# Optimization experiments

Hardware: AMD Instinct MI355X
Metric: run time of the kernel (lower is better)

Reference implementation:

```python
import jax, jax.numpy as jnp
import numpy as np

EPS = 1e-8

def _cosine_rows(a, b):
    na = jnp.maximum(jnp.linalg.norm(a, axis=1), EPS)
    nb = jnp.maximum(jnp.linalg.norm(b, axis=1), EPS)
    return jnp.sum(a * b, axis=1) / (na * nb)


def setup_inputs() -> dict:
    key = jax.random.key(0)
    k1, k2 = jax.random.split(key)
    X = jax.random.normal(k1, (16384, 1024), dtype=jnp.float32)
    dictionary = jax.random.normal(k2, (4096, 1024), dtype=jnp.float32)
    descriptors = jnp.arange(4096, dtype=jnp.int64)
    return {"X": X, "dictionary": dictionary, "descriptors": descriptors, "k": 16}


def reference(X, dictionary, descriptors, k):
    # SOMP with centering=True, criterion='l1', pc=None (default forward path)
    orig_X = X
    std_orig_sum = jnp.sum(jnp.var(orig_X, axis=0, ddof=1))
    X_mean = jnp.mean(X, axis=0, keepdims=True)   # [1, D]
    Xc = X - X_mean                               # centered data [N, D]

    M = dictionary.shape[0]
    notchosen = jnp.ones((M,), dtype=X.dtype)
    residual = Xc
    chosen, evr, l2, cosine = [], [], [], []
    W = None
    recon = jnp.zeros_like(Xc)

    for i in range(k):  # k is a static Python int -> unrolled, per-step shapes static
        cross = residual @ dictionary.T           # [N, M] -- dominant memory traffic
        scores = jnp.sum(jnp.abs(cross * notchosen), axis=0)  # l1 criterion
        idx = jnp.argmax(scores)
        chosen.append(idx)
        notchosen = notchosen.at[idx].set(0)

        atoms = dictionary[jnp.stack(chosen)]     # [i+1, D], dynamic gather, static shape
        # least squares: min ||atoms.T @ W - Xc.T||  (full column rank -> normal eqs)
        G = atoms @ atoms.T                       # [i+1, i+1]
        W = jnp.linalg.solve(G, atoms @ Xc.T)     # [i+1, N]
        recon = (atoms.T @ W).T                   # [N, D]
        residual = Xc - recon

        rec_full = X_mean + recon
        evr.append(jnp.sum(jnp.var(rec_full, axis=0, ddof=1)) / std_orig_sum)
        cosine.append(jnp.mean(_cosine_rows(orig_X, rec_full)))
        l2.append(jnp.mean((orig_X - rec_full) ** 2))

    weights = jnp.linalg.norm(W, axis=1)          # [k]
    chosen_arr = jnp.stack(chosen)
    recon_out = X_mean + recon
    residual_out = Xc - recon                     # == X - recon_out
    return (recon_out, residual_out, chosen_arr, weights, W.T,
            jnp.stack(evr), jnp.stack(l2), jnp.stack(cosine))
```

## Files before the change

### kernel.cpp

```cpp
#include <hip/hip_runtime.h>
#include <math.h>

#define NROWS 16384
#define DIMK  1024
#define MDIC  4096
#define KSEL  16

#define OFF_RECON   0
#define OFF_RESID   ((size_t)NROWS*DIMK)
#define OFF_CHOSEN  ((size_t)2*NROWS*DIMK)
#define OFF_WEIGHTS (OFF_CHOSEN + 16)
#define OFF_WT      (OFF_WEIGHTS + 16)
#define OFF_EVR     (OFF_WT + (size_t)NROWS*KSEL)
#define OFF_L2      (OFF_EVR + 16)
#define OFF_COS     (OFF_L2 + 16)

typedef unsigned short u16;
typedef unsigned long long u64;
typedef __attribute__((ext_vector_type(8))) short short8;
typedef __attribute__((ext_vector_type(4))) float f32x4;

__device__ inline float blockReduce256f(float v) {
    __shared__ float ws_[4];
    #pragma unroll
    for (int off = 32; off > 0; off >>= 1) v += __shfl_down(v, off);
    __syncthreads();
    if ((threadIdx.x & 63) == 0) ws_[threadIdx.x >> 6] = v;
    __syncthreads();
    return ws_[0] + ws_[1] + ws_[2] + ws_[3];
}

__device__ inline void wredStore(double v, int k, int lane, int wv, double (*accS)[4]) {
    #pragma unroll
    for (int off = 32; off > 0; off >>= 1) v += __shfl_down(v, off);
    if (lane == 0) accS[k][wv] = v;
}

__device__ inline u16 f2bf(float f) {
    unsigned u = __float_as_uint(f);
    unsigned r = u + 0x7FFFu + ((u >> 16) & 1u);
    return (u16)(r >> 16);
}
__device__ inline float bf2f(u16 h) { return __uint_as_float(((unsigned)h) << 16); }

__global__ void k_init(float* notchosen, u64* amx, u64* statsAcc, u64* ctr2) {
    int m = blockIdx.x * 256 + threadIdx.x;
    if (m < MDIC) notchosen[m] = 1.0f;
    if (blockIdx.x == 0) {
        if (threadIdx.x < 40) statsAcc[threadIdx.x] = 0ULL;
        if (threadIdx.x < 2)  amx[threadIdx.x] = 0ULL;
        if (threadIdx.x == 0) *ctr2 = 0ULL;
    }
}

__global__ __launch_bounds__(256) void k_colstats(const float* __restrict__ X,
                                                  float* __restrict__ colpart,
                                                  float* __restrict__ sqpart) {
    int d  = blockIdx.x * 256 + threadIdx.x;
    int r0 = blockIdx.y * 256;
    float s = 0.f, sq = 0.f;
    for (int r = 0; r < 256; ++r) {
        float v = X[(size_t)(r0 + r) * DIMK + d];
        s += v; sq += v * v;
    }
    colpart[(size_t)blockIdx.y * DIMK + d] = s;
    __shared__ float red[256];
    red[threadIdx.x] = sq; __syncthreads();
    for (int off = 128; off > 0; off >>= 1) {
        if (threadIdx.x < off) red[threadIdx.x] += red[threadIdx.x + off];
        __syncthreads();
    }
    if (threadIdx.x == 0) sqpart[blockIdx.y * 4 + blockIdx.x] = red[0];
}

__global__ __launch_bounds__(1024) void k_reduce_mean(const float* __restrict__ colpart,
                                                      const float* __restrict__ sqpart,
                                                      float* __restrict__ xmean,
                                                      double* __restrict__ scal) {
    int d = threadIdx.x;
    double s = 0.0;
    for (int y = 0; y < 64; ++y) s += (double)colpart[(size_t)y * DIMK + d];
    float m = (float)(s / (double)NROWS);
    xmean[d] = m;
    __shared__ double red[1024];
    red[d] = (double)m * (double)m; __syncthreads();
    for (int off = 512; off > 0; off >>= 1) {
        if (d < off) red[d] += red[d + off];
        __syncthreads();
    }
    if (d == 0) {
        double xmn2 = red[0];
        double sx2 = 0.0;
        for (int i = 0; i < 256; ++i) sx2 += (double)sqpart[i];
        scal[0] = sx2;
        scal[1] = sx2 - (double)NROWS * xmn2;
        scal[2] = xmn2;
    }
}

__global__ __launch_bounds__(256) void k_md(const float* __restrict__ Dict,
                                            const float* __restrict__ xmean,
                                            float* __restrict__ md,
                                            float* __restrict__ Dnorm2) {
    int m = blockIdx.x, t = threadIdx.x;
    float4 a = ((const float4*)(Dict + (size_t)m * DIMK))[t];
    float4 b = ((const float4*)xmean)[t];
    float s  = a.x * b.x + a.y * b.y + a.z * b.z + a.w * b.w;
    float sn = a.x * a.x + a.y * a.y + a.z * a.z + a.w * a.w;
    s  = blockReduce256f(s);
    sn = blockReduce256f(sn);
    if (t == 0) { md[m] = s; Dnorm2[m] = sn; }
}

__global__ __launch_bounds__(256) void k_split(const float* __restrict__ src,
                                               u16* __restrict__ hi,
                                               u16* __restrict__ lo) {
    size_t idx = ((size_t)blockIdx.x * 256 + threadIdx.x) * 4;
    float4 v = *(const float4*)(src + idx);
    ushort4 h, l;
    h.x = f2bf(v.x); l.x = f2bf(v.x - bf2f(h.x));
    h.y = f2bf(v.y); l.y = f2bf(v.y - bf2f(h.y));
    h.z = f2bf(v.z); l.z = f2bf(v.z - bf2f(h.z));
    h.w = f2bf(v.w); l.w = f2bf(v.w - bf2f(h.w));
    *(ushort4*)(hi + idx) = h;
    *(ushort4*)(lo + idx) = l;
}

__global__ __launch_bounds__(256) void k_splitX(const float* __restrict__ src,
                                                u16* __restrict__ hi,
                                                u16* __restrict__ lo,
                                                const float* __restrict__ xmean,
                                                float* __restrict__ Xnorm2,
                                                float* __restrict__ XdotM) {
    int n = blockIdx.x, t = threadIdx.x;
    size_t idx = (size_t)n * DIMK + t * 4;
    float4 v = *(const float4*)(src + idx);
    float4 mv = ((const float4*)xmean)[t];
    ushort4 h, l;
    h.x = f2bf(v.x); l.x = f2bf(v.x - bf2f(h.x));
    h.y = f2bf(v.y); l.y = f2bf(v.y - bf2f(h.y));
    h.z = f2bf(v.z); l.z = f2bf(v.z - bf2f(h.z));
    h.w = f2bf(v.w); l.w = f2bf(v.w - bf2f(h.w));
    *(ushort4*)(hi + idx) = h;
    *(ushort4*)(lo + idx) = l;
    float s2 = v.x * v.x + v.y * v.y + v.z * v.z + v.w * v.w;
    float sm = v.x * mv.x + v.y * mv.y + v.z * mv.z + v.w * mv.w;
    s2 = blockReduce256f(s2);
    sm = blockReduce256f(sm);
    if (t == 0) { Xnorm2[n] = s2; XdotM[n] = sm; }
}


#define GLL16(g, l) __builtin_amdgcn_global_load_lds( \
    (__attribute__((address_space(1))) void*)(g), \
    (__attribute__((address_space(3))) void*)(l), 16, 0, 0)

#define STAGE_A2(pa_, kc_, wb_, q0_, q1_) do { \
    GLL16((pa_) + aGbase + (size_t)(q0_) * 64 * DIMK + (kc_), \
          sA + (wb_) * 16384 + (q0_) * 4096 + lWbase); \
    GLL16((pa_) + aGbase + (size_t)(q1_) * 64 * DIMK + (kc_), \
          sA + (wb_) * 16384 + (q1_) * 4096 + lWbase); \
} while (0)

#define STAGE_B2(pb_, kc_, wb_, q0_, q1_) do { \
    GLL16((pb_) + bGbase + (size_t)(q0_) * 64 * DIMK + (kc_), \
          sB + (wb_) * 16384 + (q0_) * 4096 + lWbase); \
    GLL16((pb_) + bGbase + (size_t)(q1_) * 64 * DIMK + (kc_), \
          sB + (wb_) * 16384 + (q1_) * 4096 + lWbase); \
} while (0)

#define VM2 asm volatile("s_waitcnt vmcnt(2)" ::: "memory")
#define VM0 asm volatile("s_waitcnt vmcnt(0)" ::: "memory")
#define NOPSTMT ((void)0)

#define PHASE_BA(rb_, s_, STAGE_STMT, WAIT_STMT) do { \
    const u16* pA_ = sA + (rb_) * 16384; \
    const u16* pB_ = sB + (rb_) * 16384; \
    int ko_ = (s_) ? koff1 : koff0; \
    _Pragma("unroll") \
    for (int nf = 0; nf < 4; ++nf) \
        bq[nf] = *(const short8*)&pB_[boffB + nf * 1024 + ko_]; \
    _Pragma("unroll") \
    for (int fi = 0; fi < 4; ++fi) \
        aq[fi] = *(const short8*)&pA_[aoffA + fi * 1024 + ko_]; \
    STAGE_STMT; \
    __builtin_amdgcn_s_barrier(); \
    __builtin_amdgcn_s_setprio(1); \
    _Pragma("unroll") \
    for (int fi = 0; fi < 4; ++fi) \
        _Pragma("unroll") \
        for (int nf = 0; nf < 4; ++nf) \
            acc[fi][nf] = __builtin_amdgcn_mfma_f32_16x16x32_bf16( \
                aq[fi], bq[nf], acc[fi][nf], 0, 0, 0); \
    __builtin_amdgcn_s_setprio(0); \
    WAIT_STMT; \
    __builtin_amdgcn_s_barrier(); \
} while (0)

#define PHASE_A(rb_, s_, STAGE_STMT, WAIT_STMT) do { \
    const u16* pA_ = sA + (rb_) * 16384; \
    int ko_ = (s_) ? koff1 : koff0; \
    _Pragma("unroll") \
    for (int fi = 0; fi < 4; ++fi) \
        aq[fi] = *(const short8*)&pA_[aoffA + (4 + fi) * 1024 + ko_]; \
    STAGE_STMT; \
    __builtin_amdgcn_s_barrier(); \
    __builtin_amdgcn_s_setprio(1); \
    _Pragma("unroll") \
    for (int fi = 0; fi < 4; ++fi) \
        _Pragma("unroll") \
        for (int nf = 0; nf < 4; ++nf) \
            acc[4 + fi][nf] = __builtin_amdgcn_mfma_f32_16x16x32_bf16( \
                aq[fi], bq[nf], acc[4 + fi][nf], 0, 0, 0); \
    __builtin_amdgcn_s_setprio(0); \
    WAIT_STMT; \
    __builtin_amdgcn_s_barrier(); \
} while (0)

__global__ __launch_bounds__(512, 2) void k_gemm8(const u16* __restrict__ Ahi,
                                                  const u16* __restrict__ Alo,
                                                  const u16* __restrict__ Bhi,
                                                  const u16* __restrict__ Blo,
                                                  const float* __restrict__ md,
                                                  u16* __restrict__ C0h,
                                                  int rowAbase) {
    __shared__ u16 sA[2 * 16384];
    __shared__ u16 sB[2 * 16384];
    int T = threadIdx.x;
    int lane = T & 63, wid = T >> 6;
    int wr = wid >> 2, wc = wid & 3;

    int nwg = gridDim.x, cpx = nwg >> 3;
    int bid = blockIdx.x;
    int wg  = (bid & 7) * cpx + (bid >> 3);
    int bm = wg >> 4, bn = wg & 15;
    int rowA0 = bm * 256, rowB0 = bn * 256;

    int sw = (T & 7) ^ ((T >> 3) & 7);
    size_t aGbase = (size_t)(rowA0 + (T >> 3)) * DIMK + sw * 8;
    size_t bGbase = (size_t)(rowB0 + (T >> 3)) * DIMK + sw * 8;
    int lWbase = (T >> 6) * 512;

    int lm = lane & 15, lk = lane >> 4;
    int kb0 = (lk * 16) ^ ((lane & 7) << 4);
    int kb1 = (64 + lk * 16) ^ ((lane & 7) << 4);
    int koff0 = kb0 >> 1, koff1 = kb1 >> 1;
    int aoffA = (wr * 128 + lm) * 64;
    int boffB = (wc * 64 + lm) * 64;

    f32x4 acc[8][4];
    f32x4 zero = {0.f, 0.f, 0.f, 0.f};
    #pragma unroll
    for (int i = 0; i < 8; ++i)
        #pragma unroll
        for (int j = 0; j < 4; ++j) acc[i][j] = zero;
    short8 bq[4], aq[4];

    STAGE_B2(Bhi, 0, 0, 0, 1);
    STAGE_B2(Bhi, 0, 0, 2, 3);
    STAGE_A2(Ahi, 0, 0, 0, 2);
    STAGE_A2(Ahi, 0, 0, 1, 3);
    VM2;
    __builtin_amdgcn_s_barrier();

    for (int t = 0; t < 47; ++t) {
        int rbuf = t & 1, wbuf = rbuf ^ 1;
        int kk = (t + 1) << 6;
        int seg = kk >> 10;
        const u16* pa = (seg == 1) ? Alo : Ahi;
        const u16* pb = (seg == 2) ? Blo : Bhi;
        int kc = kk & 1023;
        PHASE_BA(rbuf, 0, STAGE_B2(pb, kc, wbuf, 0, 1), VM2);
        PHASE_A (rbuf, 0, STAGE_B2(pb, kc, wbuf, 2, 3), NOPSTMT);
        PHASE_BA(rbuf, 1, STAGE_A2(pa, kc, wbuf, 0, 2), NOPSTMT);
        PHASE_A (rbuf, 1, STAGE_A2(pa, kc, wbuf, 1, 3), VM2);
    }
    PHASE_BA(1, 0, NOPSTMT, VM0);
    PHASE_A (1, 0, NOPSTMT, NOPSTMT);
    PHASE_BA(1, 1, NOPSTMT, NOPSTMT);
    PHASE_A (1, 1, NOPSTMT, NOPSTMT);

    #pragma unroll
    for (int nf = 0; nf < 4; ++nf) {
        int m = rowB0 + wc * 64 + nf * 16 + lm;
        float mdv = md[m];
        #pragma unroll
        for (int mf = 0; mf < 8; ++mf) {
            int nb = rowAbase + rowA0 + wr * 128 + mf * 16 + lk * 4;
            #pragma unroll
            for (int r = 0; r < 4; ++r)
                C0h[(size_t)(nb + r) * MDIC + m] = f2bf(acc[mf][nf][r] - mdv);
        }
    }
}

template <int NA>
__global__ __launch_bounds__(256) void k_score(const u16* __restrict__ C0h,
                                               const float* __restrict__ GR,
                                               const float* __restrict__ Wm,
                                               float* __restrict__ scorePf) {
    constexpr int NAX = NA ? NA : 1;
    __shared__ float Wl[NAX][64];
    int t = threadIdx.x;
    int m0 = blockIdx.x * 1024 + t * 4;
    int n0 = blockIdx.y * 64;
    float4 gr[NAX];
    #pragma unroll
    for (int j = 0; j < NA; ++j) gr[j] = *(const float4*)&GR[(size_t)j * MDIC + m0];
    for (int idx = t; idx < NA * 64; idx += 256) {
        int j = idx >> 6, nn = idx & 63;
        Wl[j][nn] = Wm[(size_t)j * NROWS + n0 + nn];
    }
    __syncthreads();
    float4 acc = {0.f, 0.f, 0.f, 0.f};
    for (int nn = 0; nn < 64; ++nn) {
        ushort4 ch = *(const ushort4*)&C0h[(size_t)(n0 + nn) * MDIC + m0];
        float4 c = {bf2f(ch.x), bf2f(ch.y), bf2f(ch.z), bf2f(ch.w)};
        float4 cr = {0.f, 0.f, 0.f, 0.f};
        #pragma unroll
        for (int j = 0; j < NA; ++j) {
            float wv = Wl[j][nn];
            cr.x += wv * gr[j].x; cr.y += wv * gr[j].y;
            cr.z += wv * gr[j].z; cr.w += wv * gr[j].w;
        }
        acc.x += fabsf(c.x - cr.x); acc.y += fabsf(c.y - cr.y);
        acc.z += fabsf(c.z - cr.z); acc.w += fabsf(c.w - cr.w);
    }
    *(float4*)&scorePf[(size_t)blockIdx.y * MDIC + m0] = acc;
}

__global__ __launch_bounds__(256) void k_scoreargmax(const float* __restrict__ scorePf,
                                                     float* __restrict__ notchosen,
                                                     u64* __restrict__ amx,
                                                     int* __restrict__ chosen,
                                                     float* __restrict__ outChosen,
                                                     const float* __restrict__ md,
                                                     const float* __restrict__ Dnorm2,
                                                     const float* __restrict__ GR,
                                                     float* __restrict__ Lmat,
                                                     float* __restrict__ Gcc,
                                                     float* __restrict__ mdot,
                                                     int iter) {
    int t = threadIdx.x;
    int m0 = blockIdx.x * 256;
    int tm = t & 63, yg = t >> 6;
    float sx = 0.f, sy = 0.f, sz = 0.f, sw = 0.f;
    #pragma unroll 4
    for (int y = yg; y < 256; y += 4) {
        float4 v = *(const float4*)&scorePf[(size_t)y * MDIC + m0 + (tm << 2)];
        sx += v.x; sy += v.y; sz += v.z; sw += v.w;
    }
    __shared__ float4 red4[4][64];
    float4 pv; pv.x = sx; pv.y = sy; pv.z = sz; pv.w = sw;
    red4[yg][tm] = pv;
    __syncthreads();
    u64 best = 0ULL;
    if (t < 64) {
        float4 a = red4[0][t], b = red4[1][t], cc = red4[2][t], d = red4[3][t];
        double sv[4] = {(double)a.x + b.x + cc.x + d.x,
                        (double)a.y + b.y + cc.y + d.y,
                        (double)a.z + b.z + cc.z + d.z,
                        (double)a.w + b.w + cc.w + d.w};
        int mb = m0 + (t << 2);
        #pragma unroll
        for (int j = 0; j < 4; ++j) {
            if (notchosen[mb + j] != 0.f) {
                u64 key = ((u64)__double_as_longlong(sv[j]) & ~0xFFFULL) | (u64)(4095 - (mb + j));
                if (key > best) best = key;
            }
        }
        #pragma unroll
        for (int off = 32; off > 0; off >>= 1) {
            u64 o = __shfl_down(best, off);
            if (o > best) best = o;
        }
    }
    __shared__ int slast, sc;
    if (t == 0) {
        atomicMax(&amx[0], best);
        __threadfence();
        u64 done = atomicAdd(&amx[1], 1ULL);
        slast = (done == 15ULL) ? 1 : 0;
        if (slast) {
            u64 k = atomicMax(&amx[0], 0ULL);
            int c = 4095 - (int)(k & 0xFFFULL);
            sc = c;
            chosen[iter] = c;
            notchosen[c] = 0.f;
            outChosen[iter] = (float)c;
            mdot[iter] = md[c];
            amx[0] = 0ULL; amx[1] = 0ULL;
        }
    }
    __syncthreads();
    if (!slast) return;
    int c = sc;
    __shared__ float Lsh[16][16];
    __shared__ float g[17];
    __shared__ float LrowS[16];
    Lsh[t >> 4][t & 15] = Lmat[t];
    if (t < iter)  g[t] = GR[(size_t)t * MDIC + c];
    if (t == iter) g[t] = Dnorm2[c];
    __syncthreads();
    if (t == 0) {
        for (int b = 0; b < iter; ++b) {
            float s = g[b];
            for (int x = 0; x < b; ++x) s -= LrowS[x] * Lsh[b][x];
            LrowS[b] = s / Lsh[b][b];
        }
        float s2 = g[iter];
        for (int x = 0; x < iter; ++x) s2 -= LrowS[x] * LrowS[x];
        LrowS[iter] = sqrtf(fmaxf(s2, 1e-20f));
        for (int b = 0; b <= iter; ++b) Lmat[iter * 16 + b] = LrowS[b];
        for (int b = iter + 1; b < 16; ++b) Lmat[iter * 16 + b] = 0.f;
        for (int b = 0; b < iter; ++b) { Gcc[iter * 16 + b] = g[b]; Gcc[b * 16 + iter] = g[b]; }
        Gcc[iter * 16 + iter] = g[iter];
    }
}

template <int NAT>
__global__ __launch_bounds__(256) void k_gramsolve(const float* __restrict__ Dict,
                                                   const int* __restrict__ chosen,
                                                   const u16* __restrict__ C0h,
                                                   float* __restrict__ GR,
                                                   float* __restrict__ Bm,
                                                   const float* __restrict__ Lmat,
                                                   const float* __restrict__ Gcc_g,
                                                   const float* __restrict__ mdot,
                                                   const float* __restrict__ Xnorm2,
                                                   const float* __restrict__ XdotM,
                                                   const double* __restrict__ scal,
                                                   float* __restrict__ Wm,
                                                   u64* __restrict__ statsAcc,
                                                   u64* __restrict__ ctr2,
                                                   float* __restrict__ out, int iter) {
    int t = threadIdx.x;
    int c = chosen[iter];
    if (blockIdx.x >= 64) {
        int m = blockIdx.x - 64;
        float4 a = ((const float4*)(Dict + (size_t)c * DIMK))[t];
        float4 b = ((const float4*)(Dict + (size_t)m * DIMK))[t];
        float s = a.x * b.x + a.y * b.y + a.z * b.z + a.w * b.w;
        s = blockReduce256f(s);
        if (t == 0) GR[(size_t)iter * MDIC + m] = s;
        return;
    }
    constexpr int NV = 3 + 2 * NAT;
    __shared__ float L[16][16];
    __shared__ float G[16][16];
    __shared__ float mdl[16];
    __shared__ double accS[35][4];
    if (t < NAT * NAT) {
        int a = t / NAT, b2 = t % NAT;
        L[a][b2] = Lmat[a * 16 + b2];
        G[a][b2] = Gcc_g[a * 16 + b2];
    }
    if (t < NAT) mdl[t] = mdot[t];
    __syncthreads();
    int n = blockIdx.x * 256 + t;
    float b[NAT], y[NAT], w[NAT];
    #pragma unroll
    for (int j = 0; j < NAT - 1; ++j) b[j] = Bm[(size_t)j * NROWS + n];
    float bn = bf2f(C0h[(size_t)n * MDIC + c]);
    b[NAT - 1] = bn;
    Bm[(size_t)(NAT - 1) * NROWS + n] = bn;
    #pragma unroll
    for (int a = 0; a < NAT; ++a) {
        float s = b[a];
        #pragma unroll
        for (int x = 0; x < NAT; ++x) if (x < a) s -= L[a][x] * y[x];
        y[a] = s / L[a][a];
    }
    #pragma unroll
    for (int a = NAT - 1; a >= 0; --a) {
        float s = y[a];
        #pragma unroll
        for (int x = 0; x < NAT; ++x) if (x > a) s -= L[x][a] * w[x];
        w[a] = s / L[a][a];
    }
    #pragma unroll
    for (int j = 0; j < NAT; ++j) Wm[(size_t)j * NROWS + n] = w[j];

    float q = 0.f, wb = 0.f, wmd = 0.f, num1 = 0.f;
    #pragma unroll
    for (int j = 0; j < NAT; ++j) {
        float gw = 0.f;
        #pragma unroll
        for (int x = 0; x < NAT; ++x) gw += G[j][x] * w[x];
        q    += w[j] * gw;
        wb   += w[j] * b[j];
        wmd  += w[j] * mdl[j];
        num1 += w[j] * (b[j] + mdl[j]);
    }
    float xmn2 = (float)scal[2];
    float rec2 = xmn2 + 2.f * wmd + q;
    float na = fmaxf(sqrtf(Xnorm2[n]), 1e-8f);
    float nb = fmaxf(sqrtf(fmaxf(rec2, 0.f)), 1e-8f);
    float cosn = (XdotM[n] + num1) / (na * nb);

    int lane = t & 63, wv = t >> 6;
    wredStore((double)q,    0, lane, wv, accS);
    wredStore((double)wb,   1, lane, wv, accS);
    wredStore((double)cosn, 2, lane, wv, accS);
    #pragma unroll
    for (int j = 0; j < NAT; ++j) {
        wredStore((double)w[j],                 3 + j,       lane, wv, accS);
        wredStore((double)w[j] * (double)w[j],  3 + NAT + j, lane, wv, accS);
    }
    __syncthreads();
    if (t < NV) {
        double tot = accS[t][0] + accS[t][1] + accS[t][2] + accS[t][3];
        long long fx = (long long)(tot * 1048576.0);
        atomicAdd(&statsAcc[t], (u64)fx);
    }
    __shared__ int slast2;
    __syncthreads();
    if (t == 0) {
        __threadfence();
        slast2 = (atomicAdd(ctr2, 1ULL) == 63ULL) ? 1 : 0;
    }
    __syncthreads();
    if (!slast2) return;
    __shared__ double stot[35];
    __shared__ double wbarS[16];
    if (t < NV) {
        u64 raw = atomicAdd(&statsAcc[t], 0ULL);
        stot[t] = (double)(long long)raw * (1.0 / 1048576.0);
        statsAcc[t] = 0ULL;
    }
    if (t == 0) *ctr2 = 0ULL;
    __syncthreads();
    if (t < NAT) wbarS[t] = stot[3 + t] * (1.0 / (double)NROWS);
    __syncthreads();
    if (t == 0) {
        double q2 = stot[0], wb2 = stot[1], cs = stot[2];
        double wg = 0.0;
        for (int a = 0; a < NAT; ++a)
            for (int b2 = 0; b2 < NAT; ++b2) wg += wbarS[a] * wbarS[b2] * (double)G[a][b2];
        double sumXc2 = scal[1];
        out[OFF_EVR + iter] = (float)((q2 - (double)NROWS * wg) / sumXc2);
        out[OFF_L2  + iter] = (float)((sumXc2 - 2.0 * wb2 + q2) / ((double)NROWS * (double)DIMK));
        out[OFF_COS + iter] = (float)(cs / (double)NROWS);
        if (NAT == KSEL) {
            for (int j = 0; j < NAT; ++j)
                out[OFF_WEIGHTS + j] = (float)sqrt(stot[3 + NAT + j]);
        }
    }
}

__global__ __launch_bounds__(256) void k_outfinal(const float* __restrict__ X,
                                                  const float* __restrict__ xmean,
                                                  const float* __restrict__ Dict,
                                                  const int* __restrict__ chosen,
                                                  const float* __restrict__ Wm,
                                                  float* __restrict__ out) {
    __shared__ int cI[16];
    int t = threadIdx.x;
    if (t < 16) cI[t] = chosen[t];
    __syncthreads();
    int n0 = blockIdx.x * 8;
    if (t < 128) {
        int j = t & 15, r = t >> 4;
        int n = n0 + r;
        out[OFF_WT + (size_t)n * 16 + j] = Wm[(size_t)j * NROWS + n];
    }
    float4 xm = ((const float4*)xmean)[t];
    for (int r = 0; r < 8; ++r) {
        int n = n0 + r;
        float w[16];
        #pragma unroll
        for (int j = 0; j < 16; ++j) w[j] = Wm[(size_t)j * NROWS + n];
        float4 rec = xm;
        #pragma unroll
        for (int j = 0; j < 16; ++j) {
            float4 a = ((const float4*)(Dict + (size_t)cI[j] * DIMK))[t];
            rec.x += w[j] * a.x; rec.y += w[j] * a.y;
            rec.z += w[j] * a.z; rec.w += w[j] * a.w;
        }
        float4 xv = ((const float4*)(X + (size_t)n * DIMK))[t];
        float4 res = {xv.x - rec.x, xv.y - rec.y, xv.z - rec.z, xv.w - rec.w};
        ((float4*)(out + OFF_RECON + (size_t)n * DIMK))[t] = rec;
        ((float4*)(out + OFF_RESID + (size_t)n * DIMK))[t] = res;
    }
}

struct IterArgs {
    const float *X, *Dict;
    u16 *C0h;
    float *GR, *W, *Bm, *md, *Dnorm2, *xmean, *Xnorm2, *XdotM, *notchosen, *Lmat, *Gcc, *mdot;
    float *scorePf;
    u64 *amx, *statsAcc, *ctr2;
    double *scal;
    int *chosen;
    float *out;
    hipStream_t stream;
};

template <int I>
static void run_iter(const IterArgs& a) {
    k_score<I><<<dim3(4, 256), 256, 0, a.stream>>>(a.C0h, a.GR, a.W, a.scorePf);
    k_scoreargmax<<<16, 256, 0, a.stream>>>(a.scorePf, a.notchosen, a.amx, a.chosen,
                                            a.out + OFF_CHOSEN, a.md, a.Dnorm2, a.GR,
                                            a.Lmat, a.Gcc, a.mdot, I);
    k_gramsolve<I + 1><<<MDIC + 64, 256, 0, a.stream>>>(a.Dict, a.chosen, a.C0h, a.GR,
                                                        a.Bm, a.Lmat, a.Gcc, a.mdot,
                                                        a.Xnorm2, a.XdotM, a.scal, a.W,
                                                        a.statsAcc, a.ctr2, a.out, I);
}

template <int I>
struct Loop {
    static void go(const IterArgs& a) { run_iter<I>(a); Loop<I + 1>::go(a); }
};
template <>
struct Loop<KSEL> { static void go(const IterArgs&) {} };

extern "C" void kernel_launch(void* const* d_in, const int* in_sizes, int n_in,
                              void* d_out, int out_size, void* d_ws, size_t ws_size,
                              hipStream_t stream) {
    (void)in_sizes; (void)n_in; (void)out_size;
    const float* X    = (const float*)d_in[0];
    const float* Dict = (const float*)d_in[1];
    float* out = (float*)d_out;

    char* ws = (char*)d_ws;
    size_t off = 0;
    auto carve = [&](size_t bytes) -> char* {
        char* p = ws + off;
        off += (bytes + 255) & ~(size_t)255;
        return p;
    };
    u16*    C0h       = (u16*)   carve((size_t)NROWS * MDIC * 2);
    float*  GR        = (float*) carve((size_t)KSEL * MDIC * 4);
    float*  W         = (float*) carve((size_t)KSEL * NROWS * 4);
    float*  Bm        = (float*) carve((size_t)KSEL * NROWS * 4);
    float*  md        = (float*) carve((size_t)MDIC * 4);
    float*  Dnorm2    = (float*) carve((size_t)MDIC * 4);
    float*  xmean     = (float*) carve((size_t)DIMK * 4);
    float*  colpart   = (float*) carve((size_t)64 * DIMK * 4);
    float*  sqpart    = (float*) carve(256 * 4);
    float*  Xnorm2    = (float*) carve((size_t)NROWS * 4);
    float*  XdotM     = (float*) carve((size_t)NROWS * 4);
    float*  scorePf   = (float*) carve((size_t)256 * MDIC * 4);
    float*  notchosen = (float*) carve((size_t)MDIC * 4);
    u64*    amx       = (u64*)   carve(2 * 8);
    u64*    statsAcc  = (u64*)   carve(40 * 8);
    u64*    ctr2      = (u64*)   carve(8);
    int*    chosen    = (int*)   carve(KSEL * 4);
    float*  Lmat      = (float*) carve(256 * 4);
    float*  Gcc       = (float*) carve(256 * 4);
    float*  mdot      = (float*) carve(16 * 4);
    double* scal      = (double*)carve(8 * 8);
    u16*    Bhi       = (u16*)   carve((size_t)MDIC * DIMK * 2);
    u16*    Blo       = (u16*)   carve((size_t)MDIC * DIMK * 2);

    int chunkrows = 0;
    for (int cr = NROWS; cr >= 256; cr >>= 1) {
        size_t need = (size_t)cr * DIMK * 2 * 2 + 512;
        if (off + need <= ws_size) { chunkrows = cr; break; }
    }
    if (chunkrows == 0) chunkrows = 256;
    u16* Ahi = (u16*) carve((size_t)chunkrows * DIMK * 2);
    u16* Alo = (u16*) carve((size_t)chunkrows * DIMK * 2);

    k_init<<<MDIC / 256, 256, 0, stream>>>(notchosen, amx, statsAcc, ctr2);
    k_colstats<<<dim3(4, 64), 256, 0, stream>>>(X, colpart, sqpart);
    k_reduce_mean<<<1, 1024, 0, stream>>>(colpart, sqpart, xmean, scal);
    k_md<<<MDIC, 256, 0, stream>>>(Dict, xmean, md, Dnorm2);

    k_split<<<(MDIC * DIMK) / 1024, 256, 0, stream>>>(Dict, Bhi, Blo);
    int nchunks = NROWS / chunkrows;
    for (int c = 0; c < nchunks; ++c) {
        k_splitX<<<chunkrows, 256, 0, stream>>>(
            X + (size_t)c * chunkrows * DIMK, Ahi, Alo, xmean,
            Xnorm2 + (size_t)c * chunkrows, XdotM + (size_t)c * chunkrows);
        int mtiles = chunkrows / 256;
        k_gemm8<<<dim3(mtiles * 16), 512, 0, stream>>>(
            Ahi, Alo, Bhi, Blo, md, C0h, c * chunkrows);
    }

    IterArgs a{X, Dict, C0h, GR, W, Bm, md, Dnorm2, xmean, Xnorm2, XdotM, notchosen,
               Lmat, Gcc, mdot, scorePf, amx, statsAcc, ctr2, scal, chosen, out, stream};
    Loop<0>::go(a);

    k_outfinal<<<NROWS / 8, 256, 0, stream>>>(X, xmean, Dict, chosen, W, out);
}
```

Measured before the change: 1.476 ms.

## Fuse score and argmax kernels via last-blocks ticket; restage GEMM loads

The per-iteration score kernel and the separate argmax kernel are merged. Each block takes a ticket from an atomic counter, and the last 16 blocks spin until all blocks finish, then do the column reduction and argmax. This removes one kernel launch per iteration, sixteen in total. Separately, the GEMM main loop now issues all A and B tile loads in the first two phases with vmcnt(4)/vmcnt(0) waits, instead of spreading them over four phases. The spin-wait depends on the last-ticketed blocks not blocking earlier ones, and the front-loaded loads may cut overlap between loads and MFMA work.

```diff
diff --git a/kernel.cpp b/kernel.cpp
--- a/kernel.cpp
+++ b/kernel.cpp
@@ -5,6 +5,7 @@
 #define DIMK  1024
 #define MDIC  4096
 #define KSEL  16
+#define NBLK_SCORE 1024
 
 #define OFF_RECON   0
 #define OFF_RESID   ((size_t)NROWS*DIMK)
@@ -43,13 +44,13 @@
 }
 __device__ inline float bf2f(u16 h) { return __uint_as_float(((unsigned)h) << 16); }
 
-__global__ void k_init(float* notchosen, u64* amx, u64* statsAcc, u64* ctr2) {
+__global__ void k_init(float* notchosen, u64* amx, u64* statsAcc, u64* ctr2, u64* ctr3) {
     int m = blockIdx.x * 256 + threadIdx.x;
     if (m < MDIC) notchosen[m] = 1.0f;
     if (blockIdx.x == 0) {
         if (threadIdx.x < 40) statsAcc[threadIdx.x] = 0ULL;
         if (threadIdx.x < 2)  amx[threadIdx.x] = 0ULL;
-        if (threadIdx.x == 0) *ctr2 = 0ULL;
+        if (threadIdx.x == 0) { *ctr2 = 0ULL; *ctr3 = 0ULL; }
     }
 }
 
@@ -155,20 +156,21 @@
     (__attribute__((address_space(1))) void*)(g), \
     (__attribute__((address_space(3))) void*)(l), 16, 0, 0)
 
-#define STAGE_A2(pa_, kc_, wb_, q0_, q1_) do { \
-    GLL16((pa_) + aGbase + (size_t)(q0_) * 64 * DIMK + (kc_), \
-          sA + (wb_) * 16384 + (q0_) * 4096 + lWbase); \
-    GLL16((pa_) + aGbase + (size_t)(q1_) * 64 * DIMK + (kc_), \
-          sA + (wb_) * 16384 + (q1_) * 4096 + lWbase); \
+#define STAGE_A4(pa_, kc_, wb_) do { \
+    GLL16((pa_) + aGbase + (size_t)0 * 64 * DIMK + (kc_), sA + (wb_) * 16384 + 0 * 4096 + lWbase); \
+    GLL16((pa_) + aGbase + (size_t)2 * 64 * DIMK + (kc_), sA + (wb_) * 16384 + 2 * 4096 + lWbase); \
+    GLL16((pa_) + aGbase + (size_t)1 * 64 * DIMK + (kc_), sA + (wb_) * 16384 + 1 * 4096 + lWbase); \
+    GLL16((pa_) + aGbase + (size_t)3 * 64 * DIMK + (kc_), sA + (wb_) * 16384 + 3 * 4096 + lWbase); \
 } while (0)
 
-#define STAGE_B2(pb_, kc_, wb_, q0_, q1_) do { \
-    GLL16((pb_) + bGbase + (size_t)(q0_) * 64 * DIMK + (kc_), \
-          sB + (wb_) * 16384 + (q0_) * 4096 + lWbase); \
-    GLL16((pb_) + bGbase + (size_t)(q1_) * 64 * DIMK + (kc_), \
-          sB + (wb_) * 16384 + (q1_) * 4096 + lWbase); \
+#define STAGE_B4(pb_, kc_, wb_) do { \
+    GLL16((pb_) + bGbase + (size_t)0 * 64 * DIMK + (kc_), sB + (wb_) * 16384 + 0 * 4096 + lWbase); \
+    GLL16((pb_) + bGbase + (size_t)1 * 64 * DIMK + (kc_), sB + (wb_) * 16384 + 1 * 4096 + lWbase); \
+    GLL16((pb_) + bGbase + (size_t)2 * 64 * DIMK + (kc_), sB + (wb_) * 16384 + 2 * 4096 + lWbase); \
+    GLL16((pb_) + bGbase + (size_t)3 * 64 * DIMK + (kc_), sB + (wb_) * 16384 + 3 * 4096 + lWbase); \
 } while (0)
 
+#define VM4 asm volatile("s_waitcnt vmcnt(4)" ::: "memory")
 #define VM2 asm volatile("s_waitcnt vmcnt(2)" ::: "memory")
 #define VM0 asm volatile("s_waitcnt vmcnt(0)" ::: "memory")
 #define NOPSTMT ((void)0)
@@ -256,10 +258,11 @@
         for (int j = 0; j < 4; ++j) acc[i][j] = zero;
     short8 bq[4], aq[4];
 
-    STAGE_B2(Bhi, 0, 0, 0, 1);
-    STAGE_B2(Bhi, 0, 0, 2, 3);
-    STAGE_A2(Ahi, 0, 0, 0, 2);
-    STAGE_A2(Ahi, 0, 0, 1, 3);
+    STAGE_B4(Bhi, 0, 0);
+    GLL16(Ahi + aGbase + (size_t)0 * 64 * DIMK, sA + 0 * 4096 + lWbase);
+    GLL16(Ahi + aGbase + (size_t)2 * 64 * DIMK, sA + 2 * 4096 + lWbase);
+    GLL16(Ahi + aGbase + (size_t)1 * 64 * DIMK, sA + 1 * 4096 + lWbase);
+    GLL16(Ahi + aGbase + (size_t)3 * 64 * DIMK, sA + 3 * 4096 + lWbase);
     VM2;
     __builtin_amdgcn_s_barrier();
 
@@ -270,12 +273,12 @@
         const u16* pa = (seg == 1) ? Alo : Ahi;
         const u16* pb = (seg == 2) ? Blo : Bhi;
         int kc = kk & 1023;
-        PHASE_BA(rbuf, 0, STAGE_B2(pb, kc, wbuf, 0, 1), VM2);
-        PHASE_A (rbuf, 0, STAGE_B2(pb, kc, wbuf, 2, 3), NOPSTMT);
-        PHASE_BA(rbuf, 1, STAGE_A2(pa, kc, wbuf, 0, 2), NOPSTMT);
-        PHASE_A (rbuf, 1, STAGE_A2(pa, kc, wbuf, 1, 3), VM2);
-    }
-    PHASE_BA(1, 0, NOPSTMT, VM0);
+        PHASE_BA(rbuf, 0, STAGE_B4(pb, kc, wbuf), VM4);
+        PHASE_A (rbuf, 0, STAGE_A4(pa, kc, wbuf), NOPSTMT);
+        PHASE_BA(rbuf, 1, NOPSTMT, VM4);
+        PHASE_A (rbuf, 1, NOPSTMT, VM0);
+    }
+    PHASE_BA(1, 0, NOPSTMT, NOPSTMT);
     PHASE_A (1, 0, NOPSTMT, NOPSTMT);
     PHASE_BA(1, 1, NOPSTMT, NOPSTMT);
     PHASE_A (1, 1, NOPSTMT, NOPSTMT);
@@ -295,10 +298,21 @@
 }
 
 template <int NA>
-__global__ __launch_bounds__(256) void k_score(const u16* __restrict__ C0h,
-                                               const float* __restrict__ GR,
-                                               const float* __restrict__ Wm,
-                                               float* __restrict__ scorePf) {
+__global__ __launch_bounds__(256) void k_scorefused(const u16* __restrict__ C0h,
+                                                    const float* __restrict__ GR,
+                                                    const float* __restrict__ Wm,
+                                                    float* __restrict__ scorePf,
+                                                    float* __restrict__ notchosen,
+                                                    u64* __restrict__ amx,
+                                                    u64* __restrict__ ctr3,
+                                                    int* __restrict__ chosen,
+                                                    float* __restrict__ outChosen,
+                                                    const float* __restrict__ md,
+                                                    const float* __restrict__ Dnorm2,
+                                                    float* __restrict__ Lmat,
+                                                    float* __restrict__ Gcc,
+                                                    float* __restrict__ mdot,
+                                                    int iter) {
     constexpr int NAX = NA ? NA : 1;
     __shared__ float Wl[NAX][64];
     int t = threadIdx.x;
@@ -327,27 +341,29 @@
         acc.z += fabsf(c.z - cr.z); acc.w += fabsf(c.w - cr.w);
     }
     *(float4*)&scorePf[(size_t)blockIdx.y * MDIC + m0] = acc;
-}
-
-__global__ __launch_bounds__(256) void k_scoreargmax(const float* __restrict__ scorePf,
-                                                     float* __restrict__ notchosen,
-                                                     u64* __restrict__ amx,
-                                                     int* __restrict__ chosen,
-                                                     float* __restrict__ outChosen,
-                                                     const float* __restrict__ md,
-                                                     const float* __restrict__ Dnorm2,
-                                                     const float* __restrict__ GR,
-                                                     float* __restrict__ Lmat,
-                                                     float* __restrict__ Gcc,
-                                                     float* __restrict__ mdot,
-                                                     int iter) {
-    int t = threadIdx.x;
-    int m0 = blockIdx.x * 256;
+
+    __shared__ int sTicket;
+    __syncthreads();
+    if (t == 0) {
+        __threadfence();
+        sTicket = (int)atomicAdd(ctr3, 1ULL);
+    }
+    __syncthreads();
+    if (sTicket < NBLK_SCORE - 16) return;
+    int slice = sTicket - (NBLK_SCORE - 16);
+
+    if (t == 0) {
+        while (atomicAdd(ctr3, 0ULL) < (u64)NBLK_SCORE) __builtin_amdgcn_s_sleep(2);
+        __threadfence();
+    }
+    __syncthreads();
+
+    int ms = slice * 256;
     int tm = t & 63, yg = t >> 6;
     float sx = 0.f, sy = 0.f, sz = 0.f, sw = 0.f;
     #pragma unroll 4
     for (int y = yg; y < 256; y += 4) {
-        float4 v = *(const float4*)&scorePf[(size_t)y * MDIC + m0 + (tm << 2)];
+        float4 v = *(const float4*)&scorePf[(size_t)y * MDIC + ms + (tm << 2)];
         sx += v.x; sy += v.y; sz += v.z; sw += v.w;
     }
     __shared__ float4 red4[4][64];
@@ -361,7 +377,7 @@
                         (double)a.y + b.y + cc.y + d.y,
                         (double)a.z + b.z + cc.z + d.z,
                         (double)a.w + b.w + cc.w + d.w};
-        int mb = m0 + (t << 2);
+        int mb = ms + (t << 2);
         #pragma unroll
         for (int j = 0; j < 4; ++j) {
             if (notchosen[mb + j] != 0.f) {
@@ -390,6 +406,7 @@
             outChosen[iter] = (float)c;
             mdot[iter] = md[c];
             amx[0] = 0ULL; amx[1] = 0ULL;
+            *ctr3 = 0ULL;
         }
     }
     __syncthreads();
@@ -589,7 +606,7 @@
     u16 *C0h;
     float *GR, *W, *Bm, *md, *Dnorm2, *xmean, *Xnorm2, *XdotM, *notchosen, *Lmat, *Gcc, *mdot;
     float *scorePf;
-    u64 *amx, *statsAcc, *ctr2;
+    u64 *amx, *statsAcc, *ctr2, *ctr3;
     double *scal;
     int *chosen;
     float *out;
@@ -598,10 +615,9 @@
 
 template <int I>
 static void run_iter(const IterArgs& a) {
-    k_score<I><<<dim3(4, 256), 256, 0, a.stream>>>(a.C0h, a.GR, a.W, a.scorePf);
-    k_scoreargmax<<<16, 256, 0, a.stream>>>(a.scorePf, a.notchosen, a.amx, a.chosen,
-                                            a.out + OFF_CHOSEN, a.md, a.Dnorm2, a.GR,
-                                            a.Lmat, a.Gcc, a.mdot, I);
+    k_scorefused<I><<<dim3(4, 256), 256, 0, a.stream>>>(
+        a.C0h, a.GR, a.W, a.scorePf, a.notchosen, a.amx, a.ctr3, a.chosen,
+        a.out + OFF_CHOSEN, a.md, a.Dnorm2, a.Lmat, a.Gcc, a.mdot, I);
     k_gramsolve<I + 1><<<MDIC + 64, 256, 0, a.stream>>>(a.Dict, a.chosen, a.C0h, a.GR,
                                                         a.Bm, a.Lmat, a.Gcc, a.mdot,
                                                         a.Xnorm2, a.XdotM, a.scal, a.W,
@@ -646,6 +662,7 @@
     u64*    amx       = (u64*)   carve(2 * 8);
     u64*    statsAcc  = (u64*)   carve(40 * 8);
     u64*    ctr2      = (u64*)   carve(8);
+    u64*    ctr3      = (u64*)   carve(8);
     int*    chosen    = (int*)   carve(KSEL * 4);
     float*  Lmat      = (float*) carve(256 * 4);
     float*  Gcc       = (float*) carve(256 * 4);
@@ -663,7 +680,7 @@
     u16* Ahi = (u16*) carve((size_t)chunkrows * DIMK * 2);
     u16* Alo = (u16*) carve((size_t)chunkrows * DIMK * 2);
 
-    k_init<<<MDIC / 256, 256, 0, stream>>>(notchosen, amx, statsAcc, ctr2);
+    k_init<<<MDIC / 256, 256, 0, stream>>>(notchosen, amx, statsAcc, ctr2, ctr3);
     k_colstats<<<dim3(4, 64), 256, 0, stream>>>(X, colpart, sqpart);
     k_reduce_mean<<<1, 1024, 0, stream>>>(colpart, sqpart, xmean, scal);
     k_md<<<MDIC, 256, 0, stream>>>(Dict, xmean, md, Dnorm2);
@@ -680,7 +697,7 @@
     }
 
     IterArgs a{X, Dict, C0h, GR, W, Bm, md, Dnorm2, xmean, Xnorm2, XdotM, notchosen,
-               Lmat, Gcc, mdot, scorePf, amx, statsAcc, ctr2, scal, chosen, out, stream};
+               Lmat, Gcc, mdot, scorePf, amx, statsAcc, ctr2, ctr3, scal, chosen, out, stream};
     Loop<0>::go(a);
 
     k_outfinal<<<NROWS / 8, 256, 0, stream>>>(X, xmean, Dict, chosen, W, out);
```

New measurement: 1.972 ms. 1.34x slower.
